# Optimization experiments

Measured on AMD Instinct MI355X. Metric: run time of the kernel, lower is better.

## Reference

```python
import jax, jax.numpy as jnp
import numpy as np

B, S, D, H = 32, 4096, 128, 8

def setup_inputs() -> dict:
    key = jax.random.key(0)
    kx, kkq, kv = jax.random.split(key, 3)
    x = jax.random.normal(kx, (B, S, D), dtype=jnp.float32)
    # nn.Linear weights: y = x @ W.T, weight shape [D, D]; stacked over heads.
    W_kq = jax.random.normal(kkq, (H, D, D), dtype=jnp.float32)
    W_v = jax.random.normal(kv, (H, D, D), dtype=jnp.float32)
    return {"x": x, "W_kq": W_kq, "W_v": W_v}


def reference(x, W_kq, W_v):
    # Original per-head math:
    #   kq_h = x @ W_kq[h].T                      [B,S,D]
    #   scores_h = x @ kq_h^T = x @ W_kq[h] @ x^T [B,S,S]
    #   out_h = scores_h @ (x @ W_v[h].T)
    # Reassociated (identical math, linear in S):
    #   out = x @ (sum_h W_kq[h] @ (x^T x) @ W_v[h].T)
    G = jnp.einsum('bsd,bse->bde', x, x)              # [B,D,D] = x^T x
    M = jnp.einsum('hde,bef,hgf->bdg', W_kq, G, W_v)  # sum over heads h
    out = jnp.einsum('bsd,bdg->bsg', x, M)            # [B,S,D]
    return out
```

## Files before the change

kernel.cpp:

```cpp
#include <hip/hip_runtime.h>
#include <hip/hip_bf16.h>

#define BB 32
#define SS 4096
#define DD 128
#define HH 8

typedef __attribute__((ext_vector_type(8))) short short8;
typedef __attribute__((ext_vector_type(4))) float f32x4;
typedef unsigned long long u64;

__device__ inline unsigned short f2b(float f){
  unsigned int u = __float_as_uint(f);
  return (unsigned short)((u + 0x7fffu + ((u >> 16) & 1u)) >> 16);
}

__device__ inline int swzi(int r, int c){
  return (r << 7) | (((c >> 3) ^ (r & 7)) << 3) | (c & 7);
}

__device__ inline short8 ldfrag(const short* buf, int row, int kblk){
  return *reinterpret_cast<const short8*>(&buf[(row << 7) | ((kblk ^ (row & 7)) << 3)]);
}

__device__ inline short8 ldxfrag(const float* __restrict__ base, int row, int kblk){
  const float4* p = reinterpret_cast<const float4*>(base) + row * 32 + kblk * 2;
  float4 a = p[0], b = p[1];
  short8 r;
  r[0] = (short)f2b(a.x); r[1] = (short)f2b(a.y); r[2] = (short)f2b(a.z); r[3] = (short)f2b(a.w);
  r[4] = (short)f2b(b.x); r[5] = (short)f2b(b.y); r[6] = (short)f2b(b.z); r[7] = (short)f2b(b.w);
  return r;
}

__device__ inline void wave_gemm32x64(const short* bufA, const short* bufB,
                                      int wm, int wn, int lane, f32x4 acc[2][4]){
  #pragma unroll
  for (int ks = 0; ks < 4; ++ks){
    int kblk = ks * 4 + (lane >> 4);
    short8 af[2], bf[4];
    #pragma unroll
    for (int mt = 0; mt < 2; ++mt) af[mt] = ldfrag(bufA, wm + mt * 16 + (lane & 15), kblk);
    #pragma unroll
    for (int nt = 0; nt < 4; ++nt) bf[nt] = ldfrag(bufB, wn + nt * 16 + (lane & 15), kblk);
    #pragma unroll
    for (int mt = 0; mt < 2; ++mt)
      #pragma unroll
      for (int nt = 0; nt < 4; ++nt)
        acc[mt][nt] = __builtin_amdgcn_mfma_f32_16x16x32_bf16(af[mt], bf[nt], acc[mt][nt], 0, 0, 0);
  }
}

__device__ inline u64 packb4(float a, float b, float c, float d){
  return (u64)f2b(a) | ((u64)f2b(b) << 16) | ((u64)f2b(c) << 32) | ((u64)f2b(d) << 48);
}

template<int NT>
__device__ inline void stage128(const float* __restrict__ src, short* dst, int t){
  const float4* s4 = reinterpret_cast<const float4*>(src);
  #pragma unroll
  for (int f4 = t; f4 < 4096; f4 += NT){
    int r = f4 >> 5, c = (f4 & 31) << 2;
    float4 v = s4[f4];
    *reinterpret_cast<u64*>(&dst[swzi(r, c)]) = packb4(v.x, v.y, v.z, v.w);
  }
}

__device__ inline void ld128(const float* __restrict__ src, int t, float4 r[8]){
  const float4* s4 = reinterpret_cast<const float4*>(src);
  #pragma unroll
  for (int i = 0; i < 8; ++i) r[i] = s4[t + i * 512];
}
__device__ inline void wr128(short* dst, int t, const float4 r[8]){
  #pragma unroll
  for (int i = 0; i < 8; ++i){
    int f4 = t + i * 512;
    int rr = f4 >> 5, c = (f4 & 31) << 2;
    *reinterpret_cast<u64*>(&dst[swzi(rr, c)]) = packb4(r[i].x, r[i].y, r[i].z, r[i].w);
  }
}

__global__ __launch_bounds__(512) void k_gram(const float* __restrict__ x, float* __restrict__ Gp){
  __shared__ short xsT[128 * 128];
  const int t = threadIdx.x, lane = t & 63, wid = t >> 6;
  const int slot = blockIdx.x, b = blockIdx.y;
  const int e = t & 127, sg = t >> 7;
  const int wm = (wid >> 1) * 32, wn = (wid & 1) * 64;

  f32x4 acc[2][4];
  const f32x4 z = {0.f, 0.f, 0.f, 0.f};
  #pragma unroll
  for (int i = 0; i < 2; ++i)
    #pragma unroll
    for (int j = 0; j < 4; ++j) acc[i][j] = z;

  const float* xb = x + ((size_t)b * SS + slot * 512) * DD;
  float r0[16], r1[16];
  #pragma unroll
  for (int i = 0; i < 16; ++i){
    int s2 = sg + 4 * i;
    r0[i] = xb[(2 * s2) * DD + e];
    r1[i] = xb[(2 * s2 + 1) * DD + e];
  }
  for (int c = 0; c < 4; ++c){
    __syncthreads();
    #pragma unroll
    for (int i = 0; i < 16; ++i){
      int s2 = sg + 4 * i;
      unsigned int w = (unsigned)f2b(r0[i]) | ((unsigned)f2b(r1[i]) << 16);
      *reinterpret_cast<unsigned int*>(&xsT[swzi(e, 2 * s2)]) = w;
    }
    if (c < 3){
      const float* src = xb + (size_t)(c + 1) * 128 * DD;
      #pragma unroll
      for (int i = 0; i < 16; ++i){
        int s2 = sg + 4 * i;
        r0[i] = src[(2 * s2) * DD + e];
        r1[i] = src[(2 * s2 + 1) * DD + e];
      }
    }
    __syncthreads();
    wave_gemm32x64(xsT, xsT, wm, wn, lane, acc);
  }

  float* Gb = Gp + (size_t)(slot * BB + b) * (DD * DD);
  #pragma unroll
  for (int mt = 0; mt < 2; ++mt)
    #pragma unroll
    for (int nt = 0; nt < 4; ++nt)
      #pragma unroll
      for (int i = 0; i < 4; ++i){
        int ee = wm + mt * 16 + ((lane >> 4) << 2) + i;
        int ff = wn + nt * 16 + (lane & 15);
        Gb[(ee << 7) + ff] = acc[mt][nt][i];
      }
}

__global__ __launch_bounds__(256) void k_gsum(const float* __restrict__ Gp, short* __restrict__ Gbf){
  const int id = blockIdx.x * 256 + threadIdx.x;
  const float4* g4 = reinterpret_cast<const float4*>(Gp);
  #pragma unroll
  for (int it = 0; it < 4; ++it){
    int F = id + it * 32768;
    int b = F >> 12, j4 = F & 4095;
    float4 s = {0.f, 0.f, 0.f, 0.f};
    #pragma unroll
    for (int sl = 0; sl < 8; ++sl){
      float4 v = g4[(size_t)(sl * BB + b) * 4096 + j4];
      s.x += v.x; s.y += v.y; s.z += v.z; s.w += v.w;
    }
    int r = j4 >> 5, c = (j4 & 31) << 2;
    *reinterpret_cast<u64*>(&Gbf[(size_t)b * 16384 + swzi(r, c)]) = packb4(s.x, s.y, s.z, s.w);
  }
}

__global__ __launch_bounds__(512) void k_heads(const short* __restrict__ Gbf,
                                               const float* __restrict__ Wkq,
                                               const float* __restrict__ Wv,
                                               float* __restrict__ Mp){
  __shared__ short bufW[128 * 128];
  __shared__ short bufG[128 * 128];
  __shared__ short bufT[128 * 128];
  const int t = threadIdx.x, lane = t & 63, wid = t >> 6;
  const int h = blockIdx.x, b = blockIdx.y;
  const int wm = (wid >> 1) * 32, wn = (wid & 1) * 64;
  const f32x4 z = {0.f, 0.f, 0.f, 0.f};

  stage128<512>(Wv + (size_t)h * DD * DD, bufW, t);
  {
    const short8* g8 = reinterpret_cast<const short8*>(Gbf + (size_t)b * 16384);
    short8* d8 = reinterpret_cast<short8*>(bufG);
    #pragma unroll
    for (int i = 0; i < 4; ++i) d8[t + i * 512] = g8[t + i * 512];
  }
  __syncthreads();

  float4 wk[8];
  ld128(Wkq + (size_t)h * DD * DD, t, wk);

  f32x4 acc[2][4];
  #pragma unroll
  for (int i = 0; i < 2; ++i)
    #pragma unroll
    for (int j = 0; j < 4; ++j) acc[i][j] = z;
  wave_gemm32x64(bufW, bufG, wm, wn, lane, acc);
  __syncthreads();

  #pragma unroll
  for (int mt = 0; mt < 2; ++mt)
    #pragma unroll
    for (int nt = 0; nt < 4; ++nt)
      #pragma unroll
      for (int i = 0; i < 4; ++i){
        int g = wm + mt * 16 + ((lane >> 4) << 2) + i;
        int e = wn + nt * 16 + (lane & 15);
        bufT[swzi(g, e)] = (short)f2b(acc[mt][nt][i]);
      }
  wr128(bufW, t, wk);
  __syncthreads();

  #pragma unroll
  for (int i = 0; i < 2; ++i)
    #pragma unroll
    for (int j = 0; j < 4; ++j) acc[i][j] = z;
  wave_gemm32x64(bufT, bufW, wm, wn, lane, acc);

  float* Mb = Mp + (size_t)(h * BB + b) * (DD * DD);
  #pragma unroll
  for (int mt = 0; mt < 2; ++mt)
    #pragma unroll
    for (int nt = 0; nt < 4; ++nt)
      #pragma unroll
      for (int i = 0; i < 4; ++i){
        int g = wm + mt * 16 + ((lane >> 4) << 2) + i;
        int d = wn + nt * 16 + (lane & 15);
        Mb[(g << 7) + d] = acc[mt][nt][i];
      }
}

__global__ __launch_bounds__(256) void k_red(const float* __restrict__ Mp, short* __restrict__ Mb){
  const int id = blockIdx.x * 256 + threadIdx.x;
  const float4* p4 = reinterpret_cast<const float4*>(Mp);
  u64* o8 = reinterpret_cast<u64*>(Mb);
  #pragma unroll
  for (int it = 0; it < 4; ++it){
    int F = id + it * 32768;
    int b = F >> 12, j4 = F & 4095;
    float4 s = {0.f, 0.f, 0.f, 0.f};
    #pragma unroll
    for (int hh = 0; hh < 8; ++hh){
      float4 v = p4[(size_t)(hh * BB + b) * 4096 + j4];
      s.x += v.x; s.y += v.y; s.z += v.z; s.w += v.w;
    }
    o8[F] = packb4(s.x, s.y, s.z, s.w);
  }
}

__global__ __launch_bounds__(512) void k_out(const float* __restrict__ x,
                                             const short* __restrict__ Mbf,
                                             float* __restrict__ out){
  __shared__ short bufM[128 * 128];
  const int t = threadIdx.x, lane = t & 63, wid = t >> 6;
  const int b = blockIdx.y, s0 = blockIdx.x * 256;
  const int wm = (wid >> 1) * 32, wn = (wid & 1) * 64;
  const f32x4 z = {0.f, 0.f, 0.f, 0.f};

  {
    const short8* m8 = reinterpret_cast<const short8*>(Mbf + (size_t)b * DD * DD);
    #pragma unroll
    for (int i = 0; i < 4; ++i){
      int idx = t + i * 512;
      int r = idx >> 4, c8 = idx & 15;
      *reinterpret_cast<short8*>(&bufM[(r << 7) | ((c8 ^ (r & 7)) << 3)]) = m8[idx];
    }
  }
  __syncthreads();

  const float* xb = x + ((size_t)b * SS + s0) * DD;
  #pragma unroll
  for (int c = 0; c < 2; ++c){
    f32x4 acc[2][4];
    #pragma unroll
    for (int i = 0; i < 2; ++i)
      #pragma unroll
      for (int j = 0; j < 4; ++j) acc[i][j] = z;

    #pragma unroll
    for (int ks = 0; ks < 4; ++ks){
      int kblk = ks * 4 + (lane >> 4);
      short8 af[2], bf[4];
      #pragma unroll
      for (int mt = 0; mt < 2; ++mt)
        af[mt] = ldxfrag(xb, c * 128 + wm + mt * 16 + (lane & 15), kblk);
      #pragma unroll
      for (int nt = 0; nt < 4; ++nt) bf[nt] = ldfrag(bufM, wn + nt * 16 + (lane & 15), kblk);
      #pragma unroll
      for (int mt = 0; mt < 2; ++mt)
        #pragma unroll
        for (int nt = 0; nt < 4; ++nt)
          acc[mt][nt] = __builtin_amdgcn_mfma_f32_16x16x32_bf16(af[mt], bf[nt], acc[mt][nt], 0, 0, 0);
    }

    float* ob = out + ((size_t)b * SS + s0 + c * 128) * DD;
    #pragma unroll
    for (int mt = 0; mt < 2; ++mt)
      #pragma unroll
      for (int nt = 0; nt < 4; ++nt)
        #pragma unroll
        for (int i = 0; i < 4; ++i){
          int sp = wm + mt * 16 + ((lane >> 4) << 2) + i;
          int g = wn + nt * 16 + (lane & 15);
          ob[(sp << 7) + g] = acc[mt][nt][i];
        }
  }
}

extern "C" void kernel_launch(void* const* d_in, const int* in_sizes, int n_in,
                              void* d_out, int out_size, void* d_ws, size_t ws_size,
                              hipStream_t stream) {
  const float* x   = (const float*)d_in[0];
  const float* Wkq = (const float*)d_in[1];
  const float* Wv  = (const float*)d_in[2];
  float* out = (float*)d_out;

  float* Gp  = (float*)d_ws;
  float* Mp  = Gp + (size_t)8 * BB * DD * DD;
  short* Gbf = (short*)(Mp + (size_t)HH * BB * DD * DD);
  short* Mb  = Gbf + (size_t)BB * DD * DD;

  k_gram <<<dim3(8, BB),        512, 0, stream>>>(x, Gp);
  k_gsum <<<dim3(128),          256, 0, stream>>>(Gp, Gbf);
  k_heads<<<dim3(HH, BB),       512, 0, stream>>>(Gbf, Wkq, Wv, Mp);
  k_red  <<<dim3(128),          256, 0, stream>>>(Mp, Mb);
  k_out  <<<dim3(SS / 256, BB), 512, 0, stream>>>(x, Mb, out);
}
```

Measured before the change: 152.2 us.

## Split head kernel rows across two blocks and widen gram LDS transpose stores

The per-head kernel now splits the 128 output rows into two 64-row halves handled by separate blocks. This doubles the grid from 256 to 512 blocks and shrinks LDS per block from three 32KB buffers to 16KB+32KB, which should raise occupancy and parallelism. Each half block still re-stages the full G and Wkq, so that global/LDS traffic is duplicated. Separately, the gram kernel's transposed bf16 stores into LDS now write 8 consecutive s values as one 16-byte short8 instead of 32-bit pairs, cutting LDS store instructions at the cost of more register-held values per thread.

```diff
diff --git a/kernel.cpp b/kernel.cpp
--- a/kernel.cpp
+++ b/kernel.cpp
@@ -50,15 +50,33 @@
   }
 }
 
+__device__ inline void wave_gemm32x32(const short* bufA, const short* bufB,
+                                      int wm, int wn, int lane, f32x4 acc[2][2]){
+  #pragma unroll
+  for (int ks = 0; ks < 4; ++ks){
+    int kblk = ks * 4 + (lane >> 4);
+    short8 af[2], bf[2];
+    #pragma unroll
+    for (int mt = 0; mt < 2; ++mt) af[mt] = ldfrag(bufA, wm + mt * 16 + (lane & 15), kblk);
+    #pragma unroll
+    for (int nt = 0; nt < 2; ++nt) bf[nt] = ldfrag(bufB, wn + nt * 16 + (lane & 15), kblk);
+    #pragma unroll
+    for (int mt = 0; mt < 2; ++mt)
+      #pragma unroll
+      for (int nt = 0; nt < 2; ++nt)
+        acc[mt][nt] = __builtin_amdgcn_mfma_f32_16x16x32_bf16(af[mt], bf[nt], acc[mt][nt], 0, 0, 0);
+  }
+}
+
 __device__ inline u64 packb4(float a, float b, float c, float d){
   return (u64)f2b(a) | ((u64)f2b(b) << 16) | ((u64)f2b(c) << 32) | ((u64)f2b(d) << 48);
 }
 
-template<int NT>
-__device__ inline void stage128(const float* __restrict__ src, short* dst, int t){
+template<int R>
+__device__ inline void stageR(const float* __restrict__ src, short* dst, int t){
   const float4* s4 = reinterpret_cast<const float4*>(src);
   #pragma unroll
-  for (int f4 = t; f4 < 4096; f4 += NT){
+  for (int f4 = t; f4 < R * 32; f4 += 512){
     int r = f4 >> 5, c = (f4 & 31) << 2;
     float4 v = s4[f4];
     *reinterpret_cast<u64*>(&dst[swzi(r, c)]) = packb4(v.x, v.y, v.z, v.w);
@@ -83,7 +101,7 @@
   __shared__ short xsT[128 * 128];
   const int t = threadIdx.x, lane = t & 63, wid = t >> 6;
   const int slot = blockIdx.x, b = blockIdx.y;
-  const int e = t & 127, sg = t >> 7;
+  const int e = t & 127, sb0 = t >> 7;
   const int wm = (wid >> 1) * 32, wn = (wid & 1) * 64;
 
   f32x4 acc[2][4];
@@ -94,29 +112,30 @@
     for (int j = 0; j < 4; ++j) acc[i][j] = z;
 
   const float* xb = x + ((size_t)b * SS + slot * 512) * DD;
-  float r0[16], r1[16];
-  #pragma unroll
-  for (int i = 0; i < 16; ++i){
-    int s2 = sg + 4 * i;
-    r0[i] = xb[(2 * s2) * DD + e];
-    r1[i] = xb[(2 * s2 + 1) * DD + e];
-  }
+  float v[4][8];
+  #pragma unroll
+  for (int i = 0; i < 4; ++i)
+    #pragma unroll
+    for (int j = 0; j < 8; ++j)
+      v[i][j] = xb[(size_t)(((sb0 + 4 * i) * 8 + j)) * DD + e];
+
   for (int c = 0; c < 4; ++c){
     __syncthreads();
     #pragma unroll
-    for (int i = 0; i < 16; ++i){
-      int s2 = sg + 4 * i;
-      unsigned int w = (unsigned)f2b(r0[i]) | ((unsigned)f2b(r1[i]) << 16);
-      *reinterpret_cast<unsigned int*>(&xsT[swzi(e, 2 * s2)]) = w;
+    for (int i = 0; i < 4; ++i){
+      int sb = sb0 + 4 * i;
+      short8 w;
+      #pragma unroll
+      for (int j = 0; j < 8; ++j) w[j] = (short)f2b(v[i][j]);
+      *reinterpret_cast<short8*>(&xsT[(e << 7) | ((sb ^ (e & 7)) << 3)]) = w;
     }
     if (c < 3){
       const float* src = xb + (size_t)(c + 1) * 128 * DD;
       #pragma unroll
-      for (int i = 0; i < 16; ++i){
-        int s2 = sg + 4 * i;
-        r0[i] = src[(2 * s2) * DD + e];
-        r1[i] = src[(2 * s2 + 1) * DD + e];
-      }
+      for (int i = 0; i < 4; ++i)
+        #pragma unroll
+        for (int j = 0; j < 8; ++j)
+          v[i][j] = src[(size_t)(((sb0 + 4 * i) * 8 + j)) * DD + e];
     }
     __syncthreads();
     wave_gemm32x64(xsT, xsT, wm, wn, lane, acc);
@@ -145,8 +164,8 @@
     float4 s = {0.f, 0.f, 0.f, 0.f};
     #pragma unroll
     for (int sl = 0; sl < 8; ++sl){
-      float4 v = g4[(size_t)(sl * BB + b) * 4096 + j4];
-      s.x += v.x; s.y += v.y; s.z += v.z; s.w += v.w;
+      float4 vv = g4[(size_t)(sl * BB + b) * 4096 + j4];
+      s.x += vv.x; s.y += vv.y; s.z += vv.z; s.w += vv.w;
     }
     int r = j4 >> 5, c = (j4 & 31) << 2;
     *reinterpret_cast<u64*>(&Gbf[(size_t)b * 16384 + swzi(r, c)]) = packb4(s.x, s.y, s.z, s.w);
@@ -157,18 +176,17 @@
                                                const float* __restrict__ Wkq,
                                                const float* __restrict__ Wv,
                                                float* __restrict__ Mp){
-  __shared__ short bufW[128 * 128];
-  __shared__ short bufG[128 * 128];
-  __shared__ short bufT[128 * 128];
+  __shared__ short bufA[64 * 128];
+  __shared__ short bufB[128 * 128];
   const int t = threadIdx.x, lane = t & 63, wid = t >> 6;
-  const int h = blockIdx.x, b = blockIdx.y;
-  const int wm = (wid >> 1) * 32, wn = (wid & 1) * 64;
+  const int h = blockIdx.x >> 1, gh = blockIdx.x & 1, b = blockIdx.y;
+  const int wm = (wid >> 2) * 32, wn = (wid & 3) * 32;
   const f32x4 z = {0.f, 0.f, 0.f, 0.f};
 
-  stage128<512>(Wv + (size_t)h * DD * DD, bufW, t);
+  stageR<64>(Wv + (size_t)h * DD * DD + (size_t)gh * 64 * DD, bufA, t);
   {
     const short8* g8 = reinterpret_cast<const short8*>(Gbf + (size_t)b * 16384);
-    short8* d8 = reinterpret_cast<short8*>(bufG);
+    short8* d8 = reinterpret_cast<short8*>(bufB);
     #pragma unroll
     for (int i = 0; i < 4; ++i) d8[t + i * 512] = g8[t + i * 512];
   }
@@ -177,38 +195,38 @@
   float4 wk[8];
   ld128(Wkq + (size_t)h * DD * DD, t, wk);
 
-  f32x4 acc[2][4];
+  f32x4 acc[2][2];
   #pragma unroll
   for (int i = 0; i < 2; ++i)
     #pragma unroll
-    for (int j = 0; j < 4; ++j) acc[i][j] = z;
-  wave_gemm32x64(bufW, bufG, wm, wn, lane, acc);
+    for (int j = 0; j < 2; ++j) acc[i][j] = z;
+  wave_gemm32x32(bufA, bufB, wm, wn, lane, acc);
   __syncthreads();
 
   #pragma unroll
   for (int mt = 0; mt < 2; ++mt)
     #pragma unroll
-    for (int nt = 0; nt < 4; ++nt)
+    for (int nt = 0; nt < 2; ++nt)
       #pragma unroll
       for (int i = 0; i < 4; ++i){
         int g = wm + mt * 16 + ((lane >> 4) << 2) + i;
         int e = wn + nt * 16 + (lane & 15);
-        bufT[swzi(g, e)] = (short)f2b(acc[mt][nt][i]);
+        bufA[swzi(g, e)] = (short)f2b(acc[mt][nt][i]);
       }
-  wr128(bufW, t, wk);
+  wr128(bufB, t, wk);
   __syncthreads();
 
   #pragma unroll
   for (int i = 0; i < 2; ++i)
     #pragma unroll
-    for (int j = 0; j < 4; ++j) acc[i][j] = z;
-  wave_gemm32x64(bufT, bufW, wm, wn, lane, acc);
-
-  float* Mb = Mp + (size_t)(h * BB + b) * (DD * DD);
+    for (int j = 0; j < 2; ++j) acc[i][j] = z;
+  wave_gemm32x32(bufA, bufB, wm, wn, lane, acc);
+
+  float* Mb = Mp + (size_t)(h * BB + b) * (DD * DD) + (size_t)gh * 64 * DD;
   #pragma unroll
   for (int mt = 0; mt < 2; ++mt)
     #pragma unroll
-    for (int nt = 0; nt < 4; ++nt)
+    for (int nt = 0; nt < 2; ++nt)
       #pragma unroll
       for (int i = 0; i < 4; ++i){
         int g = wm + mt * 16 + ((lane >> 4) << 2) + i;
@@ -228,8 +246,8 @@
     float4 s = {0.f, 0.f, 0.f, 0.f};
     #pragma unroll
     for (int hh = 0; hh < 8; ++hh){
-      float4 v = p4[(size_t)(hh * BB + b) * 4096 + j4];
-      s.x += v.x; s.y += v.y; s.z += v.z; s.w += v.w;
+      float4 vv = p4[(size_t)(hh * BB + b) * 4096 + j4];
+      s.x += vv.x; s.y += vv.y; s.z += vv.z; s.w += vv.w;
     }
     o8[F] = packb4(s.x, s.y, s.z, s.w);
   }
@@ -309,7 +327,7 @@
 
   k_gram <<<dim3(8, BB),        512, 0, stream>>>(x, Gp);
   k_gsum <<<dim3(128),          256, 0, stream>>>(Gp, Gbf);
-  k_heads<<<dim3(HH, BB),       512, 0, stream>>>(Gbf, Wkq, Wv, Mp);
+  k_heads<<<dim3(2 * HH, BB),   512, 0, stream>>>(Gbf, Wkq, Wv, Mp);
   k_red  <<<dim3(128),          256, 0, stream>>>(Mp, Mb);
   k_out  <<<dim3(SS / 256, BB), 512, 0, stream>>>(x, Mb, out);
 }
```

Result: no change. 149.8 us (-1.5%).
